# Optimization experiments

Measured on AMD Instinct MI355X. Metric: run time of the kernel, lower is better.

The kernel has to match this reference:

```python
import jax, jax.numpy as jnp
import numpy as np
from jax import lax

MAX_BOXES = 1000
IOU_THRESHOLD = 0.5
SCORE_THRESHOLD = 0.3
N_BOXES = 300000
N_FEAT = 85  # 4 box + 1 conf + 80 classes


def setup_inputs() -> dict:
    key = jax.random.key(0)
    inputs = jax.random.uniform(key, (N_BOXES, N_FEAT), dtype=jnp.float32)
    return {"inputs": inputs}


def _nms_indices(boxes, scores, max_boxes, iou_thr):
    """Fixed-size greedy NMS (tf.image.non_max_suppression semantics).
    Returns (idxs[max_boxes] int32, valid[max_boxes] bool). Padded slots invalid.
    Indices are non-differentiable, matching TF."""
    boxes = lax.stop_gradient(boxes)
    scores = lax.stop_gradient(scores)
    y1, x1, y2, x2 = boxes[:, 0], boxes[:, 1], boxes[:, 2], boxes[:, 3]
    areas = (y2 - y1) * (x2 - x1)

    def step(cur_scores, _):
        idx = jnp.argmax(cur_scores)
        valid = jnp.isfinite(cur_scores[idx])
        b = boxes[idx]
        iy1 = jnp.maximum(b[0], y1)
        ix1 = jnp.maximum(b[1], x1)
        iy2 = jnp.minimum(b[2], y2)
        ix2 = jnp.minimum(b[3], x2)
        inter = jnp.maximum(iy2 - iy1, 0.0) * jnp.maximum(ix2 - ix1, 0.0)
        union = areas[idx] + areas - inter
        iou = jnp.where(union > 0, inter / union, 0.0)
        suppress = (iou > iou_thr) & valid
        new_scores = jnp.where(suppress, -jnp.inf, cur_scores)
        new_scores = new_scores.at[idx].set(-jnp.inf)
        return new_scores, (idx.astype(jnp.int32), valid)

    _, (idxs, valids) = lax.scan(step, scores, None, length=max_boxes)
    return idxs, valids


def reference(inputs):
    boxes = inputs[..., 0:4]                      # [N,4]
    box_confidence = inputs[..., 4:5]             # [N,1]
    box_class_probs = inputs[..., 5:]             # [N,C]
    box_scores = box_confidence * box_class_probs # [N,C]
    box_classes = jnp.argmax(box_scores, axis=-1)        # [N]
    box_class_scores = jnp.max(box_scores, axis=-1)      # [N]
    # boolean_mask emulated by sending failing scores to -inf (fixed shape)
    keep = box_class_scores >= SCORE_THRESHOLD
    masked_scores = jnp.where(keep, box_class_scores, -jnp.inf)

    idxs, valids = _nms_indices(boxes, masked_scores, MAX_BOXES, IOU_THRESHOLD)

    out_boxes = boxes[idxs]                                  # [max_boxes,4]
    out_scores = box_class_scores[idxs][:, None]             # [max_boxes,1]
    out_classes = box_classes[idxs].astype(jnp.float32)[:, None]
    out = jnp.concatenate([out_boxes, out_classes, out_scores], axis=-1)  # [max_boxes,6]
    # zero padded (invalid) rows; original returned variable-length [k,6]
    return jnp.where(valids[:, None], out, 0.0)
```

## Files before the change

kernel.cpp:

```cpp
#include <hip/hip_runtime.h>

#define NBOX 300000
#define NFEAT 85
#define NCLS 80
#define NBUCK 4096
#define HSPLIT 16
#define CMAX 8192
#define W64 (CMAX / 64)
#define MAXKEEP 1000
#define SC_ROWS 64

typedef unsigned long long u64;
typedef float f4a __attribute__((ext_vector_type(4), aligned(16)));

__device__ __forceinline__ int bucket_of(float s) {
    int b = (int)((s - 0.3f) * (4096.0f / 0.7f));
    if (b < 0) b = 0;
    if (b > NBUCK - 1) b = NBUCK - 1;
    return b;
}

__device__ __forceinline__ bool sup_iou(float by1, float bx1, float by2, float bx2, float ba,
                                        float y1, float x1, float y2, float x2, float area) {
    float iy1 = fmaxf(by1, y1), ix1 = fmaxf(bx1, x1);
    float iy2 = fminf(by2, y2), ix2 = fminf(bx2, x2);
    float inter = fmaxf(iy2 - iy1, 0.0f) * fmaxf(ix2 - ix1, 0.0f);
    float uni = ba + area - inter;
    float iou = (uni > 0.0f) ? inter / uni : 0.0f;
    return iou > 0.5f;
}

__global__ void k_init(unsigned* __restrict__ hist16, unsigned* __restrict__ cnt,
                       int* __restrict__ meta) {
    int i = blockIdx.x * blockDim.x + threadIdx.x;
    if (i < HSPLIT * NBUCK) hist16[i] = 0u;
    if (i < NBUCK) cnt[i] = 0u;
    if (i < 16) meta[i] = 0;
}

__global__ void __launch_bounds__(256) k_scores(const float* __restrict__ in,
        float* __restrict__ scores, unsigned* __restrict__ hist16) {
    __shared__ float lds[SC_ROWS * NFEAT];
    int t = threadIdx.x;
    int lane = t & 63, wv = t >> 6;
    long long rbase = (long long)blockIdx.x * SC_ROWS;
    int rows = (NBOX - rbase < SC_ROWS) ? (int)(NBOX - rbase) : SC_ROWS;
    if (rows == SC_ROWS) {
        const float* src = in + rbase * NFEAT;
        for (int k = wv; k < 21; k += 4)
            __builtin_amdgcn_global_load_lds(
                (const __attribute__((address_space(1))) void*)(src + k * 256 + lane * 4),
                (__attribute__((address_space(3))) void*)&lds[k * 256], 16, 0, 0);
        if (t < 64) lds[5376 + t] = src[5376 + t];
    } else {
        int nfl = rows * NFEAT;
        int nf4 = nfl >> 2;
        const f4a* src4 = (const f4a*)(in + rbase * NFEAT);
        f4a* dst = (f4a*)lds;
        for (int k = t; k < nf4; k += 256) dst[k] = src4[k];
        for (int k = (nf4 << 2) + t; k < nfl; k += 256) lds[k] = in[rbase * NFEAT + k];
    }
    __syncthreads();
    unsigned* myhist = hist16 + (size_t)(blockIdx.x & (HSPLIT - 1)) * NBUCK;
    int row = t >> 2, part = t & 3;
    if (row < rows) {
        const float* r = lds + row * NFEAT;
        const float* p = r + 5 + 20 * part;
        float mx = p[0];
        #pragma unroll
        for (int j = 1; j < 20; ++j) mx = fmaxf(mx, p[j]);
        mx = fmaxf(mx, __shfl_xor(mx, 1));
        mx = fmaxf(mx, __shfl_xor(mx, 2));
        if (part == 0) {
            float best = r[4] * mx;
            scores[rbase + row] = best;
            if (best >= 0.3f) atomicAdd(&myhist[bucket_of(best)], 1u);
        }
    }
}

__global__ void __launch_bounds__(1024) k_thresh(const unsigned* __restrict__ hist16,
        unsigned* __restrict__ histsum, unsigned* __restrict__ off, int* __restrict__ meta) {
    __shared__ unsigned chunk[1024];
    int t = threadIdx.x;
    unsigned h[4];
    unsigned s = 0;
    #pragma unroll
    for (int j = 0; j < 4; ++j) {
        unsigned v = 0;
        for (int g = 0; g < HSPLIT; ++g) v += hist16[g * NBUCK + t * 4 + j];
        h[j] = v; histsum[t * 4 + j] = v; s += v;
    }
    chunk[t] = s;
    __syncthreads();
    for (int o = 1; o < 1024; o <<= 1) {
        unsigned add = (t + o < 1024) ? chunk[t + o] : 0u;
        __syncthreads();
        chunk[t] += add;
        __syncthreads();
    }
    unsigned after = (t + 1 < 1024) ? chunk[t + 1] : 0u;
    unsigned suf[5];
    suf[4] = after;
    #pragma unroll
    for (int j = 3; j >= 0; --j) suf[j] = suf[j + 1] + h[j];
    #pragma unroll
    for (int j = 0; j < 4; ++j) {
        int b = t * 4 + j;
        off[b] = suf[j] - h[j];
        unsigned sufb = suf[j], sufprev;
        if (b == 0) sufprev = 0xFFFFFFFFu;
        else if (j > 0) sufprev = suf[j - 1];
        else {
            unsigned hprev = 0;
            for (int g = 0; g < HSPLIT; ++g) hprev += hist16[g * NBUCK + b - 1];
            sufprev = sufb + hprev;
        }
        if (sufb <= (unsigned)CMAX && sufprev > (unsigned)CMAX) {
            meta[1] = b;
            meta[0] = (int)sufb;
        }
    }
}

__global__ void k_scatter(const float* __restrict__ scores, const int* __restrict__ meta,
                          const unsigned* __restrict__ off, unsigned* __restrict__ cnt,
                          u64* __restrict__ unsorted) {
    int i = blockIdx.x * blockDim.x + threadIdx.x;
    if (i >= NBOX) return;
    float s = scores[i];
    if (s < 0.3f) return;
    int b = bucket_of(s);
    if (b < meta[1]) return;
    unsigned slot = off[b] + atomicAdd(&cnt[b], 1u);
    if (slot < CMAX)
        unsorted[slot] = ((u64)__float_as_uint(s) << 32) |
                         (u64)(0xFFFFFFFFu - (unsigned)i);
}

__global__ void k_rank(const float* __restrict__ in, const u64* __restrict__ unsorted,
                       const unsigned* __restrict__ off, const unsigned* __restrict__ histsum,
                       const int* __restrict__ meta, u64* __restrict__ sorted,
                       float4* __restrict__ boxes4, unsigned* __restrict__ vflag) {
    int i = blockIdx.x * blockDim.x + threadIdx.x;
    int total = meta[0];
    if (i >= total) return;
    u64 k = unsorted[i];
    float s = __uint_as_float((unsigned)(k >> 32));
    int b = bucket_of(s);
    unsigned base = off[b];
    unsigned n = histsum[b];
    unsigned r = 0;
    for (unsigned u = 0; u < n; ++u) r += (unsorted[base + u] > k) ? 1u : 0u;
    int bi = (int)(0xFFFFFFFFu - (unsigned)(k & 0xFFFFFFFFull));
    const float* p = in + (size_t)bi * NFEAT;
    float4 bx = make_float4(p[0], p[1], p[2], p[3]);
    sorted[base + r] = k;
    boxes4[base + r] = bx;
    vflag[base + r] = (bx.z > bx.x && bx.w > bx.y) ? 1u : 0u;
}

__global__ void __launch_bounds__(1024) k_nms(const float4* __restrict__ boxes4,
        const unsigned* __restrict__ vflag, int* __restrict__ meta,
        unsigned* __restrict__ vincl, unsigned* __restrict__ cmap,
        float4* __restrict__ cboxes, int* __restrict__ kfinal) {
    __shared__ float4 klist[MAXKEEP + 64];
    __shared__ u64 colmask[64];
    __shared__ u64 pf[16];
    __shared__ u64 vkeptw[W64];
    __shared__ unsigned wsum[16];
    __shared__ int sh_nkept, sh_wlim, sh_stop;
    int t = threadIdx.x;
    int lane = t & 63, wv = t >> 6;
    int total = meta[0];

    if (t < W64) vkeptw[t] = 0ull;
    if (t == 0) { sh_nkept = 0; sh_wlim = 0; sh_stop = 0; }

    unsigned f[8];
    {
        unsigned run = 0;
        #pragma unroll
        for (int e = 0; e < 8; ++e) {
            int s = t * 8 + e;
            unsigned v = (s < total) ? vflag[s] : 0u;
            run += v;
            f[e] = run;
        }
        unsigned wx = run;
        #pragma unroll
        for (int o = 1; o < 64; o <<= 1) {
            unsigned u = __shfl_up(wx, o);
            if (lane >= o) wx += u;
        }
        if (lane == 63) wsum[wv] = wx;
        __syncthreads();
        if (t < 16) {
            unsigned v = wsum[t];
            #pragma unroll
            for (int o = 1; o < 16; o <<= 1) {
                unsigned u = __shfl_up(v, o);
                if (t >= o) v += u;
            }
            wsum[t] = v;
        }
        __syncthreads();
        unsigned base = ((wv > 0) ? wsum[wv - 1] : 0u) + (wx - run);
        #pragma unroll
        for (int e = 0; e < 8; ++e) {
            int s = t * 8 + e;
            unsigned incl = base + f[e];
            vincl[s] = incl;
            if (s < total && vflag[s]) {
                cmap[incl - 1] = (unsigned)s;
                cboxes[incl - 1] = boxes4[s];
            }
        }
    }
    int nv = (int)wsum[15];
    if (t == 0) meta[3] = nv;
    int nblkv = (nv + 63) >> 6;
    __syncthreads();

    for (int w = 0; w < nblkv; ++w) {
        int base = w << 6;
        int c = base + lane;
        float4 mb = (c < nv) ? cboxes[c] : make_float4(0.f, 0.f, 0.f, 0.f);
        float marea = (mb.z - mb.x) * (mb.w - mb.y);
        int cend = (base + 63 < nv - 1) ? (base + 63) : (nv - 1);
        unsigned cm = 0;
        if (wv == 0) cm = cmap[cend];
        int nk = sh_nkept;
        bool ok = true;
        for (int k = wv; k < nk; k += 16) {
            float4 b = klist[k];
            float ba = (b.z - b.x) * (b.w - b.y);
            if (sup_iou(b.x, b.y, b.z, b.w, ba, mb.x, mb.y, mb.z, mb.w, marea))
                ok = false;
        }
        u64 pv = __ballot(ok ? 1 : 0);
        if (lane == 0) pf[wv] = pv;
        #pragma unroll
        for (int r = 0; r < 4; ++r) {
            int i = wv * 4 + r;
            int ii = (base + i < nv) ? (base + i) : 0;
            float4 bi = cboxes[ii];
            float ba = (bi.z - bi.x) * (bi.w - bi.y);
            bool s = (lane > i) &&
                     sup_iou(bi.x, bi.y, bi.z, bi.w, ba, mb.x, mb.y, mb.z, mb.w, marea);
            u64 bm = __ballot(s ? 1 : 0);
            if (lane == 0) colmask[i] = bm;
        }
        __syncthreads();
        if (wv == 0) {
            int rc = nv - base;
            u64 vm = (rc >= 64) ? ~0ull : ((1ull << rc) - 1ull);
            u64 aliveM = vm;
            #pragma unroll
            for (int q = 0; q < 16; ++q) aliveM &= pf[q];
            u64 col = colmask[lane];
            u64 nzc = __ballot(col != 0ull);
            u64 remaining = aliveM, keptM = 0ull;
            while (remaining) {
                u64 hard = remaining & nzc;
                if (!hard) { keptM |= remaining; break; }
                int ih = __ffsll(hard) - 1;
                u64 below = remaining & ((1ull << ih) - 1ull);
                keptM |= below | (1ull << ih);
                remaining &= ~(below | (1ull << ih));
                u64 ci = __shfl(col, ih);
                remaining &= ~ci;
            }
            int nk0 = sh_nkept;
            if ((keptM >> lane) & 1ull) {
                int rank = __popcll(keptM & ((1ull << lane) - 1ull));
                klist[nk0 + rank] = mb;
            }
            if (lane == 0) {
                int kp = __popcll(keptM);
                vkeptw[w] = keptM;
                sh_nkept = nk0 + kp;
                sh_wlim = w + 1;
                if ((int)cm - cend + nk0 + kp >= MAXKEEP) sh_stop = 1;
            }
        }
        __syncthreads();
        if (sh_stop) break;
    }
    int wlim = sh_wlim;

    {
        unsigned run = 0;
        #pragma unroll
        for (int e = 0; e < 8; ++e) {
            int s = t * 8 + e;
            unsigned kept = 0u;
            if (s < total) {
                if (!vflag[s]) kept = 1u;
                else {
                    unsigned cc = vincl[s] - 1u;
                    int w = (int)(cc >> 6);
                    if (w < wlim && ((vkeptw[w] >> (cc & 63u)) & 1ull)) kept = 1u;
                }
            }
            run += kept;
            f[e] = run;
        }
        unsigned wx = run;
        #pragma unroll
        for (int o = 1; o < 64; o <<= 1) {
            unsigned u = __shfl_up(wx, o);
            if (lane >= o) wx += u;
        }
        __syncthreads();
        if (lane == 63) wsum[wv] = wx;
        __syncthreads();
        if (t < 16) {
            unsigned v = wsum[t];
            #pragma unroll
            for (int o = 1; o < 16; o <<= 1) {
                unsigned u = __shfl_up(v, o);
                if (t >= o) v += u;
            }
            wsum[t] = v;
        }
        __syncthreads();
        unsigned base = ((wv > 0) ? wsum[wv - 1] : 0u) + (wx - run);
        #pragma unroll
        for (int e = 0; e < 8; ++e) {
            int s = t * 8 + e;
            unsigned kept = 0u;
            if (s < total) {
                if (!vflag[s]) kept = 1u;
                else {
                    unsigned cc = vincl[s] - 1u;
                    int w = (int)(cc >> 6);
                    if (w < wlim && ((vkeptw[w] >> (cc & 63u)) & 1ull)) kept = 1u;
                }
            }
            unsigned incl = base + f[e];
            if (kept && incl <= (unsigned)MAXKEEP) kfinal[incl - 1] = s;
        }
        if (t == 0) {
            unsigned tot = wsum[15];
            meta[2] = (int)(tot < (unsigned)MAXKEEP ? tot : (unsigned)MAXKEEP);
        }
    }
}

__global__ void __launch_bounds__(256) k_output(const float* __restrict__ in,
        const u64* __restrict__ gkeys, const int* __restrict__ meta,
        const int* __restrict__ kfinal, float* __restrict__ out) {
    int gw = (blockIdx.x * blockDim.x + threadIdx.x) >> 6;
    int lane = threadIdx.x & 63;
    if (gw >= MAXKEEP) return;
    int kc = meta[2];
    if (gw < kc) {
        int pos = kfinal[gw];
        u64 key = gkeys[pos];
        int bi = (int)(0xFFFFFFFFu - (unsigned)(key & 0xFFFFFFFFull));
        const float* row = in + (size_t)bi * NFEAT;
        float conf = row[4];
        float v0 = (lane < NCLS) ? conf * row[5 + lane] : -1.0f;
        float v1 = (lane < NCLS - 64) ? conf * row[5 + 64 + lane] : -1.0f;
        float bv = (v1 > v0) ? v1 : v0;
        int bix = (v1 > v0) ? (64 + lane) : lane;
        #pragma unroll
        for (int o = 1; o < 64; o <<= 1) {
            float ov = __shfl_xor(bv, o);
            int oi = __shfl_xor(bix, o);
            if (ov > bv || (ov == bv && oi < bix)) { bv = ov; bix = oi; }
        }
        float wv = 0.f;
        if (lane < 4) wv = row[lane];
        else if (lane == 4) wv = (float)bix;
        else wv = bv;
        if (lane < 6) out[gw * 6 + lane] = wv;
    } else {
        if (lane < 6) out[gw * 6 + lane] = 0.f;
    }
}

extern "C" void kernel_launch(void* const* d_in, const int* in_sizes, int n_in,
                              void* d_out, int out_size, void* d_ws, size_t ws_size,
                              hipStream_t stream) {
    const float* in = (const float*)d_in[0];
    float* out = (float*)d_out;
    char* ws = (char*)d_ws;
    u64* sorted = (u64*)(ws);
    int* meta = (int*)(ws + 65536);
    int* kfinal = (int*)(ws + 65600);
    unsigned* vflag = (unsigned*)(ws + 69696);
    unsigned* vincl = (unsigned*)(ws + 102464);
    unsigned* cmap = (unsigned*)(ws + 135232);
    float4* cboxes = (float4*)(ws + 168000);
    float4* boxes4 = (float4*)(ws + 300096);
    float* scores = (float*)(ws + 431168);
    unsigned* hist16 = (unsigned*)(ws + 1631168);
    unsigned* histsum = (unsigned*)(ws + 1893312);
    unsigned* cnt = (unsigned*)(ws + 1909696);
    unsigned* off = (unsigned*)(ws + 1926080);
    u64* unsorted = (u64*)(ws + 1942464);

    k_init<<<dim3(256), dim3(256), 0, stream>>>(hist16, cnt, meta);
    k_scores<<<dim3((NBOX + SC_ROWS - 1) / SC_ROWS), dim3(256), 0, stream>>>(in, scores, hist16);
    k_thresh<<<dim3(1), dim3(1024), 0, stream>>>(hist16, histsum, off, meta);
    k_scatter<<<dim3((NBOX + 255) / 256), dim3(256), 0, stream>>>(scores, meta, off, cnt, unsorted);
    k_rank<<<dim3(CMAX / 256), dim3(256), 0, stream>>>(in, unsorted, off, histsum, meta, sorted, boxes4, vflag);
    k_nms<<<dim3(1), dim3(1024), 0, stream>>>(boxes4, vflag, meta, vincl, cmap, cboxes, kfinal);
    k_output<<<dim3((MAXKEEP * 64 + 255) / 256), dim3(256), 0, stream>>>(in, sorted, meta, kfinal, out);
}
```

Before: 106.5 us.

## Fuse histogram threshold scan into scatter kernel and async-load tail row

Removes the single-block k_thresh kernel by having every scatter block redundantly reduce the split histograms and run its own prefix scan into LDS, with block 0 writing the global offsets and metadata. This eliminates one launch and a serial single-block stage between score computation and scatter. In exchange each scatter block re-reads all histogram splits, which adds substantial redundant L2 traffic. It also switches the tail element copy in the score kernel to a direct global-to-LDS load.

```diff
diff --git a/kernel.cpp b/kernel.cpp
--- a/kernel.cpp
+++ b/kernel.cpp
@@ -51,7 +51,10 @@
             __builtin_amdgcn_global_load_lds(
                 (const __attribute__((address_space(1))) void*)(src + k * 256 + lane * 4),
                 (__attribute__((address_space(3))) void*)&lds[k * 256], 16, 0, 0);
-        if (t < 64) lds[5376 + t] = src[5376 + t];
+        if (wv == 0)
+            __builtin_amdgcn_global_load_lds(
+                (const __attribute__((address_space(1))) void*)(src + 5376 + lane),
+                (__attribute__((address_space(3))) void*)&lds[5376], 4, 0, 0);
     } else {
         int nfl = rows * NFEAT;
         int nf4 = nfl >> 2;
@@ -79,35 +82,40 @@
     }
 }
 
-__global__ void __launch_bounds__(1024) k_thresh(const unsigned* __restrict__ hist16,
-        unsigned* __restrict__ histsum, unsigned* __restrict__ off, int* __restrict__ meta) {
-    __shared__ unsigned chunk[1024];
+__global__ void __launch_bounds__(256) k_scatter(const float* __restrict__ scores,
+        const unsigned* __restrict__ hist16, unsigned* __restrict__ histsum,
+        unsigned* __restrict__ off_g, int* __restrict__ meta,
+        unsigned* __restrict__ cnt, u64* __restrict__ unsorted) {
+    __shared__ unsigned off_lds[NBUCK];
+    __shared__ unsigned chunk[256];
+    __shared__ int sh_bstar;
     int t = threadIdx.x;
-    unsigned h[4];
+    unsigned h[16];
     unsigned s = 0;
     #pragma unroll
-    for (int j = 0; j < 4; ++j) {
+    for (int j = 0; j < 16; ++j) {
+        int b = t * 16 + j;
         unsigned v = 0;
-        for (int g = 0; g < HSPLIT; ++g) v += hist16[g * NBUCK + t * 4 + j];
-        h[j] = v; histsum[t * 4 + j] = v; s += v;
+        for (int g = 0; g < HSPLIT; ++g) v += hist16[g * NBUCK + b];
+        h[j] = v; s += v;
     }
     chunk[t] = s;
     __syncthreads();
-    for (int o = 1; o < 1024; o <<= 1) {
-        unsigned add = (t + o < 1024) ? chunk[t + o] : 0u;
+    for (int o = 1; o < 256; o <<= 1) {
+        unsigned add = (t + o < 256) ? chunk[t + o] : 0u;
         __syncthreads();
         chunk[t] += add;
         __syncthreads();
     }
-    unsigned after = (t + 1 < 1024) ? chunk[t + 1] : 0u;
-    unsigned suf[5];
-    suf[4] = after;
+    unsigned after = (t + 1 < 256) ? chunk[t + 1] : 0u;
+    unsigned suf[17];
+    suf[16] = after;
     #pragma unroll
-    for (int j = 3; j >= 0; --j) suf[j] = suf[j + 1] + h[j];
+    for (int j = 15; j >= 0; --j) suf[j] = suf[j + 1] + h[j];
     #pragma unroll
-    for (int j = 0; j < 4; ++j) {
-        int b = t * 4 + j;
-        off[b] = suf[j] - h[j];
+    for (int j = 0; j < 16; ++j) {
+        int b = t * 16 + j;
+        off_lds[b] = suf[j + 1];
         unsigned sufb = suf[j], sufprev;
         if (b == 0) sufprev = 0xFFFFFFFFu;
         else if (j > 0) sufprev = suf[j - 1];
@@ -117,25 +125,33 @@
             sufprev = sufb + hprev;
         }
         if (sufb <= (unsigned)CMAX && sufprev > (unsigned)CMAX) {
-            meta[1] = b;
-            meta[0] = (int)sufb;
-        }
-    }
-}
-
-__global__ void k_scatter(const float* __restrict__ scores, const int* __restrict__ meta,
-                          const unsigned* __restrict__ off, unsigned* __restrict__ cnt,
-                          u64* __restrict__ unsorted) {
-    int i = blockIdx.x * blockDim.x + threadIdx.x;
-    if (i >= NBOX) return;
-    float s = scores[i];
-    if (s < 0.3f) return;
-    int b = bucket_of(s);
-    if (b < meta[1]) return;
-    unsigned slot = off[b] + atomicAdd(&cnt[b], 1u);
-    if (slot < CMAX)
-        unsorted[slot] = ((u64)__float_as_uint(s) << 32) |
-                         (u64)(0xFFFFFFFFu - (unsigned)i);
+            sh_bstar = b;
+            if (blockIdx.x == 0) { meta[1] = b; meta[0] = (int)sufb; }
+        }
+    }
+    if (blockIdx.x == 0) {
+        #pragma unroll
+        for (int j = 0; j < 16; ++j) {
+            int b = t * 16 + j;
+            histsum[b] = h[j];
+            off_g[b] = suf[j + 1];
+        }
+    }
+    __syncthreads();
+    int bstar = sh_bstar;
+    int i = blockIdx.x * blockDim.x + t;
+    if (i < NBOX) {
+        float sc = scores[i];
+        if (sc >= 0.3f) {
+            int b = bucket_of(sc);
+            if (b >= bstar) {
+                unsigned slot = off_lds[b] + atomicAdd(&cnt[b], 1u);
+                if (slot < CMAX)
+                    unsorted[slot] = ((u64)__float_as_uint(sc) << 32) |
+                                     (u64)(0xFFFFFFFFu - (unsigned)i);
+            }
+        }
+    }
 }
 
 __global__ void k_rank(const float* __restrict__ in, const u64* __restrict__ unsorted,
@@ -404,8 +420,7 @@
 
     k_init<<<dim3(256), dim3(256), 0, stream>>>(hist16, cnt, meta);
     k_scores<<<dim3((NBOX + SC_ROWS - 1) / SC_ROWS), dim3(256), 0, stream>>>(in, scores, hist16);
-    k_thresh<<<dim3(1), dim3(1024), 0, stream>>>(hist16, histsum, off, meta);
-    k_scatter<<<dim3((NBOX + 255) / 256), dim3(256), 0, stream>>>(scores, meta, off, cnt, unsorted);
+    k_scatter<<<dim3((NBOX + 255) / 256), dim3(256), 0, stream>>>(scores, hist16, histsum, off, meta, cnt, unsorted);
     k_rank<<<dim3(CMAX / 256), dim3(256), 0, stream>>>(in, unsorted, off, histsum, meta, sorted, boxes4, vflag);
     k_nms<<<dim3(1), dim3(1024), 0, stream>>>(boxes4, vflag, meta, vincl, cmap, cboxes, kfinal);
     k_output<<<dim3((MAXKEEP * 64 + 255) / 256), dim3(256), 0, stream>>>(in, sorted, meta, kfinal, out);
```

Result: slower. 133.9 us (+25.8%).
